# Kernel optimization log

Measured on AMD Instinct MI355X. Metric: run time of the kernel, lower is better.

Reference implementation:

```python
import jax, jax.numpy as jnp
import numpy as np

# hyperparameters (from init_kwargs)
A_LOG = 1.0
B_LOG = 1.0
C_LOG = 1.0
THR = 0.5
DT = 1.0
EPS = 1e-5


@jax.custom_vjp
def spike(v_scaled):
    # Heaviside forward, fast-sigmoid surrogate backward
    return (v_scaled > 0).astype(jnp.float32)

def _spike_fwd(v_scaled):
    return spike(v_scaled), v_scaled

def _spike_bwd(v_scaled, dy):
    return (dy / (1.0 + 100.0 * jnp.abs(v_scaled)) ** 2,)

spike.defvjp(_spike_fwd, _spike_bwd)


def setup_inputs() -> dict:
    key = jax.random.key(0)
    k1, k2, k3 = jax.random.split(key, 3)
    T, B, N_IN, N_REC = 1000, 128, 256, 256
    x = jax.random.normal(k1, (T, B, N_IN), dtype=jnp.float32)
    z0 = jnp.zeros((B, N_REC), dtype=jnp.float32)
    v0 = jnp.zeros((B, N_REC), dtype=jnp.float32)
    t0 = jnp.zeros((B, N_REC), dtype=jnp.float32)
    # RandomNormal(stddev=0.01) init for input weights
    w_in = 0.01 * jax.random.normal(k2, (N_IN, N_REC), dtype=jnp.float32)
    # recurrence enabled: small random recurrent weights
    w_rec = 0.01 * jax.random.normal(k3, (N_REC, N_REC), dtype=jnp.float32)
    return {"x": x, "z0": z0, "v0": v0, "t0": t0, "w_in": w_in, "w_rec": w_rec}


def _step(carry, x_t, w_in, w_rec):
    z, v, t = carry                              # each [B, n_rec]
    i_in = x_t @ w_in + z @ w_rec                # [B, n_rec]
    h = (i_in != 0).astype(jnp.float32)          # activity flag
    new_t = t + (1.0 - h)                        # (h != 1) == 1 - h since h in {0,1}
    new_v = v * (1.0 - z)                        # reset on spike
    low_pass = (new_v > -1.0).astype(jnp.float32)
    new_v = new_v - (1.0 - low_pass) * (new_v + 1.0)   # clamp at -1
    # logarithmic leak
    cap = (jnp.exp2(jnp.abs(new_v) / C_LOG) - B_LOG) / A_LOG
    arg = jnp.minimum(DT * h * (new_t + 1.0), cap)
    new_v = new_v - jnp.sign(new_v) * C_LOG * jnp.log2(EPS + A_LOG * arg + B_LOG)
    new_v = new_v + i_in
    new_t = new_t * (1.0 - h)
    new_z = spike((new_v - THR) / THR)
    return (new_z, new_v, new_t), (new_z, new_v)


def reference(x, z0, v0, t0, w_in, w_rec):
    def step(carry, x_t):
        return _step(carry, x_t, w_in, w_rec)
    _, (zs, vs) = jax.lax.scan(step, (z0, v0, t0), x)
    return zs, vs  # each [T, B, n_rec]
```

## Files before the change

### kernel.cpp

```cpp
#include <hip/hip_runtime.h>

__global__ __launch_bounds__(256) void gemm_xw(const float* __restrict__ X,
                                               const float* __restrict__ W,
                                               float* __restrict__ Y,
                                               int M) {
    __shared__ float As[32][132];
    __shared__ float Bs[32][128];

    const int tid = threadIdx.x;
    const int mb = blockIdx.x >> 1;
    const int nb = blockIdx.x & 1;
    const int m0 = mb << 7;
    const int n0 = nb << 7;
    const int tr = (tid >> 4) << 3;
    const int tc = (tid & 15) << 3;

    float acc[8][8];
#pragma unroll
    for (int i = 0; i < 8; ++i)
#pragma unroll
        for (int j = 0; j < 8; ++j) acc[i][j] = 0.f;

    for (int kb = 0; kb < 256; kb += 32) {
#pragma unroll
        for (int i = 0; i < 4; ++i) {
            int f = tid + (i << 8);
            int row = f >> 3, kq = f & 7;
            float4 a = *(const float4*)(X + (size_t)(m0 + row) * 256 + kb + (kq << 2));
            As[(kq << 2) + 0][row] = a.x;
            As[(kq << 2) + 1][row] = a.y;
            As[(kq << 2) + 2][row] = a.z;
            As[(kq << 2) + 3][row] = a.w;
            int rowb = f >> 5, cq = f & 31;
            *(float4*)&Bs[rowb][cq << 2] =
                *(const float4*)(W + (size_t)(kb + rowb) * 256 + n0 + (cq << 2));
        }
        __syncthreads();
#pragma unroll
        for (int k = 0; k < 32; ++k) {
            float a[8], b[8];
            *(float4*)&a[0] = *(const float4*)&As[k][tr];
            *(float4*)&a[4] = *(const float4*)&As[k][tr + 4];
            *(float4*)&b[0] = *(const float4*)&Bs[k][tc];
            *(float4*)&b[4] = *(const float4*)&Bs[k][tc + 4];
#pragma unroll
            for (int i = 0; i < 8; ++i)
#pragma unroll
                for (int j = 0; j < 8; ++j)
                    acc[i][j] = fmaf(a[i], b[j], acc[i][j]);
        }
        __syncthreads();
    }
#pragma unroll
    for (int i = 0; i < 8; ++i) {
        float* yp = Y + (size_t)(m0 + tr + i) * 256 + n0 + tc;
        *(float4*)yp = make_float4(acc[i][0], acc[i][1], acc[i][2], acc[i][3]);
        *(float4*)(yp + 4) = make_float4(acc[i][4], acc[i][5], acc[i][6], acc[i][7]);
    }
}

__global__ __launch_bounds__(64) void lif_seq(const float* __restrict__ ix,
                                              const float* __restrict__ wrec,
                                              const float* __restrict__ z0,
                                              const float* __restrict__ v0,
                                              const float* __restrict__ t0,
                                              float* __restrict__ zs,
                                              float* __restrict__ vs,
                                              int T, int B) {
    const int b = blockIdx.x;
    const int lane = threadIdx.x;
    const int nbase = lane << 2;
    const size_t sb = (size_t)b * 256 + nbase;
    const size_t stride = (size_t)B * 256;

    float4 v4 = *(const float4*)(v0 + sb);
    float4 t4 = *(const float4*)(t0 + sb);
    float4 z4 = *(const float4*)(z0 + sb);
    float v[4] = {v4.x, v4.y, v4.z, v4.w};
    float t[4] = {t4.x, t4.y, t4.z, t4.w};
    float z[4] = {z4.x, z4.y, z4.z, z4.w};

    unsigned long long mk0 = __ballot(z[0] != 0.f);
    unsigned long long mk1 = __ballot(z[1] != 0.f);
    unsigned long long mk2 = __ballot(z[2] != 0.f);
    unsigned long long mk3 = __ballot(z[3] != 0.f);

    const float* ixp = ix + sb;

    auto step = [&](int ts, float4 r) {
        float ir[4] = {0.f, 0.f, 0.f, 0.f};
        if (mk0 | mk1 | mk2 | mk3) {
            unsigned long long mm;
            mm = mk0;
            while (mm) { int j = __builtin_ctzll(mm); mm &= mm - 1;
                const float4 w = *(const float4*)(wrec + ((size_t)((j << 2) + 0) << 8) + nbase);
                ir[0] += w.x; ir[1] += w.y; ir[2] += w.z; ir[3] += w.w; }
            mm = mk1;
            while (mm) { int j = __builtin_ctzll(mm); mm &= mm - 1;
                const float4 w = *(const float4*)(wrec + ((size_t)((j << 2) + 1) << 8) + nbase);
                ir[0] += w.x; ir[1] += w.y; ir[2] += w.z; ir[3] += w.w; }
            mm = mk2;
            while (mm) { int j = __builtin_ctzll(mm); mm &= mm - 1;
                const float4 w = *(const float4*)(wrec + ((size_t)((j << 2) + 2) << 8) + nbase);
                ir[0] += w.x; ir[1] += w.y; ir[2] += w.z; ir[3] += w.w; }
            mm = mk3;
            while (mm) { int j = __builtin_ctzll(mm); mm &= mm - 1;
                const float4 w = *(const float4*)(wrec + ((size_t)((j << 2) + 3) << 8) + nbase);
                ir[0] += w.x; ir[1] += w.y; ir[2] += w.z; ir[3] += w.w; }
        }

        float rr[4] = {r.x, r.y, r.z, r.w};
        float nz[4];
#pragma unroll
        for (int c = 0; c < 4; ++c) {
            float i_in = rr[c] + ir[c];
            float h = (i_in != 0.f) ? 1.f : 0.f;
            float nt = t[c] + (1.f - h);
            float nv = (z[c] != 0.f) ? 0.f : v[c];
            nv = fmaxf(nv, -1.f);
            float cap = __builtin_amdgcn_exp2f(fabsf(nv)) - 1.f;
            float arg = fminf(h * (nt + 1.f), cap);
            float L = __builtin_amdgcn_logf((1e-5f + arg) + 1.f);
            float sgn = (nv > 0.f) ? 1.f : ((nv < 0.f) ? -1.f : 0.f);
            nv = fmaf(-sgn, L, nv);
            nv = nv + i_in;
            nt = nt * (1.f - h);
            float zn = ((nv - 0.5f) > 0.f) ? 1.f : 0.f;
            v[c] = nv; t[c] = nt; z[c] = zn; nz[c] = zn;
        }
        mk0 = __ballot(nz[0] != 0.f);
        mk1 = __ballot(nz[1] != 0.f);
        mk2 = __ballot(nz[2] != 0.f);
        mk3 = __ballot(nz[3] != 0.f);

        size_t o = (size_t)ts * stride + sb;
        *(float4*)(zs + o) = make_float4(z[0], z[1], z[2], z[3]);
        *(float4*)(vs + o) = make_float4(v[0], v[1], v[2], v[3]);
    };

    float4 bufA[8], bufB[8];

#define ISSUE(BUF, C)                                                          \
    {                                                                          \
        _Pragma("unroll") for (int u = 0; u < 8; ++u) {                        \
            const float* p_ = ixp + (size_t)((C) * 8 + u) * stride;            \
            asm volatile("global_load_dwordx4 %0, %1, off"                     \
                         : "=v"(BUF[u]) : "v"(p_) : "memory");                 \
        }                                                                      \
    }

#define RUNC(BUF, K)                                                           \
    { _Pragma("unroll") for (int u = 0; u < 8; ++u) step((K) * 8 + u, BUF[u]); }

    const int NC = T >> 3;

    ISSUE(bufA, 0);
    asm volatile("s_waitcnt vmcnt(0)" ::: "memory");
    __builtin_amdgcn_sched_barrier(0);

    for (int k = 0; k < NC; ++k) {
        asm volatile("s_waitcnt vmcnt(16)" ::: "memory");
        __builtin_amdgcn_sched_barrier(0);
        int nc1 = (k + 1 < NC) ? k + 1 : NC - 1;
        if ((k & 1) == 0) {
            ISSUE(bufB, nc1);
            RUNC(bufA, k);
        } else {
            ISSUE(bufA, nc1);
            RUNC(bufB, k);
        }
    }

    for (int ts = NC << 3; ts < T; ++ts) {
        float4 r = *(const float4*)(ixp + (size_t)ts * stride);
        step(ts, r);
    }
#undef ISSUE
#undef RUNC
}

extern "C" void kernel_launch(void* const* d_in, const int* in_sizes, int n_in,
                              void* d_out, int out_size, void* d_ws, size_t ws_size,
                              hipStream_t stream) {
    const float* x    = (const float*)d_in[0];
    const float* z0   = (const float*)d_in[1];
    const float* v0   = (const float*)d_in[2];
    const float* t0   = (const float*)d_in[3];
    const float* w_in = (const float*)d_in[4];
    const float* wrec = (const float*)d_in[5];

    const int n_rec = 256;
    const int B = in_sizes[1] / n_rec;
    const int nin = in_sizes[4] / n_rec;
    const int T = in_sizes[0] / (B * nin);
    const int M = T * B;

    float* zs = (float*)d_out;
    float* vs = zs + (size_t)T * B * n_rec;
    float* ixbuf = zs;

    gemm_xw<<<dim3((M / 128) * 2), dim3(256), 0, stream>>>(x, w_in, ixbuf, M);
    lif_seq<<<dim3(B), dim3(64), 0, stream>>>(ixbuf, wrec, z0, v0, t0, zs, vs, T, B);
}
```

Measured before the change: 550.8 us.

## Replace inline-asm prefetch pipeline with compiler-scheduled double buffering and batched stores

Drops the hand-written asm loads and explicit vmcnt waits for the input-current stream and uses plain C++ double-buffered chunk loads of 8 timesteps. Output stores are collected and issued together after each chunk. Recurrent weight loads now go through an asm load that waits on vmcnt(0) right away, which keeps the outstanding counter correct but may serialize in-flight prefetches behind every spike-driven weight load. The change trades explicit latency control for compiler scheduling.

```diff
diff --git a/kernel.cpp b/kernel.cpp
--- a/kernel.cpp
+++ b/kernel.cpp
@@ -87,30 +87,38 @@
 
     const float* ixp = ix + sb;
 
-    auto step = [&](int ts, float4 r) {
+    auto wload = [&](int row) -> float4 {
+        const float* wp = wrec + ((size_t)row << 8) + nbase;
+        float4 w4;
+        asm volatile("global_load_dwordx4 %0, %1, off\n\ts_waitcnt vmcnt(0)"
+                     : "=v"(w4) : "v"(wp) : "memory");
+        return w4;
+    };
+
+    auto step = [&](float4 r, float4& zo4, float4& vo4) {
         float ir[4] = {0.f, 0.f, 0.f, 0.f};
         if (mk0 | mk1 | mk2 | mk3) {
             unsigned long long mm;
             mm = mk0;
             while (mm) { int j = __builtin_ctzll(mm); mm &= mm - 1;
-                const float4 w = *(const float4*)(wrec + ((size_t)((j << 2) + 0) << 8) + nbase);
+                float4 w = wload((j << 2) + 0);
                 ir[0] += w.x; ir[1] += w.y; ir[2] += w.z; ir[3] += w.w; }
             mm = mk1;
             while (mm) { int j = __builtin_ctzll(mm); mm &= mm - 1;
-                const float4 w = *(const float4*)(wrec + ((size_t)((j << 2) + 1) << 8) + nbase);
+                float4 w = wload((j << 2) + 1);
                 ir[0] += w.x; ir[1] += w.y; ir[2] += w.z; ir[3] += w.w; }
             mm = mk2;
             while (mm) { int j = __builtin_ctzll(mm); mm &= mm - 1;
-                const float4 w = *(const float4*)(wrec + ((size_t)((j << 2) + 2) << 8) + nbase);
+                float4 w = wload((j << 2) + 2);
                 ir[0] += w.x; ir[1] += w.y; ir[2] += w.z; ir[3] += w.w; }
             mm = mk3;
             while (mm) { int j = __builtin_ctzll(mm); mm &= mm - 1;
-                const float4 w = *(const float4*)(wrec + ((size_t)((j << 2) + 3) << 8) + nbase);
+                float4 w = wload((j << 2) + 3);
                 ir[0] += w.x; ir[1] += w.y; ir[2] += w.z; ir[3] += w.w; }
         }
 
         float rr[4] = {r.x, r.y, r.z, r.w};
-        float nz[4];
+        float nzf[4], nvf[4];
 #pragma unroll
         for (int c = 0; c < 4; ++c) {
             float i_in = rr[c] + ir[c];
@@ -125,58 +133,62 @@
             nv = fmaf(-sgn, L, nv);
             nv = nv + i_in;
             nt = nt * (1.f - h);
-            float zn = ((nv - 0.5f) > 0.f) ? 1.f : 0.f;
-            v[c] = nv; t[c] = nt; z[c] = zn; nz[c] = zn;
-        }
-        mk0 = __ballot(nz[0] != 0.f);
-        mk1 = __ballot(nz[1] != 0.f);
-        mk2 = __ballot(nz[2] != 0.f);
-        mk3 = __ballot(nz[3] != 0.f);
-
+            float zf = ((nv - 0.5f) > 0.f) ? 1.f : 0.f;
+            v[c] = nv; t[c] = nt; z[c] = zf;
+            nvf[c] = nv; nzf[c] = zf;
+        }
+        mk0 = __ballot(nzf[0] != 0.f);
+        mk1 = __ballot(nzf[1] != 0.f);
+        mk2 = __ballot(nzf[2] != 0.f);
+        mk3 = __ballot(nzf[3] != 0.f);
+        zo4 = make_float4(nzf[0], nzf[1], nzf[2], nzf[3]);
+        vo4 = make_float4(nvf[0], nvf[1], nvf[2], nvf[3]);
+    };
+
+    float4 iA[8], iB[8];
+    float4 zo[8], vo[8];
+
+    auto loadChunk = [&](float4 (&ib)[8], int c0) {
+#pragma unroll
+        for (int u = 0; u < 8; ++u) {
+            int r = c0 + u;
+            r = (r < T) ? r : T - 1;
+            ib[u] = *(const float4*)(ixp + (size_t)r * stride);
+        }
+    };
+
+    auto runChunk = [&](float4 (&ib)[8], int c0) {
+#pragma unroll
+        for (int u = 0; u < 8; ++u) step(ib[u], zo[u], vo[u]);
+        size_t ob = (size_t)c0 * stride + sb;
+#pragma unroll
+        for (int u = 0; u < 8; ++u) {
+            *(float4*)(zs + ob + (size_t)u * stride) = zo[u];
+            *(float4*)(vs + ob + (size_t)u * stride) = vo[u];
+        }
+    };
+
+    loadChunk(iA, 0);
+    int c = 0;
+    while (c + 16 <= T) {
+        loadChunk(iB, c + 8);
+        runChunk(iA, c);
+        loadChunk(iA, c + 16);
+        runChunk(iB, c + 8);
+        c += 16;
+    }
+    if (c + 8 <= T) {
+        runChunk(iA, c);
+        c += 8;
+    }
+    for (int ts = c; ts < T; ++ts) {
+        float4 r = *(const float4*)(ixp + (size_t)ts * stride);
+        float4 zz, vv;
+        step(r, zz, vv);
         size_t o = (size_t)ts * stride + sb;
-        *(float4*)(zs + o) = make_float4(z[0], z[1], z[2], z[3]);
-        *(float4*)(vs + o) = make_float4(v[0], v[1], v[2], v[3]);
-    };
-
-    float4 bufA[8], bufB[8];
-
-#define ISSUE(BUF, C)                                                          \
-    {                                                                          \
-        _Pragma("unroll") for (int u = 0; u < 8; ++u) {                        \
-            const float* p_ = ixp + (size_t)((C) * 8 + u) * stride;            \
-            asm volatile("global_load_dwordx4 %0, %1, off"                     \
-                         : "=v"(BUF[u]) : "v"(p_) : "memory");                 \
-        }                                                                      \
-    }
-
-#define RUNC(BUF, K)                                                           \
-    { _Pragma("unroll") for (int u = 0; u < 8; ++u) step((K) * 8 + u, BUF[u]); }
-
-    const int NC = T >> 3;
-
-    ISSUE(bufA, 0);
-    asm volatile("s_waitcnt vmcnt(0)" ::: "memory");
-    __builtin_amdgcn_sched_barrier(0);
-
-    for (int k = 0; k < NC; ++k) {
-        asm volatile("s_waitcnt vmcnt(16)" ::: "memory");
-        __builtin_amdgcn_sched_barrier(0);
-        int nc1 = (k + 1 < NC) ? k + 1 : NC - 1;
-        if ((k & 1) == 0) {
-            ISSUE(bufB, nc1);
-            RUNC(bufA, k);
-        } else {
-            ISSUE(bufA, nc1);
-            RUNC(bufB, k);
-        }
-    }
-
-    for (int ts = NC << 3; ts < T; ++ts) {
-        float4 r = *(const float4*)(ixp + (size_t)ts * stride);
-        step(ts, r);
-    }
-#undef ISSUE
-#undef RUNC
+        *(float4*)(zs + o) = zz;
+        *(float4*)(vs + o) = vv;
+    }
 }
 
 extern "C" void kernel_launch(void* const* d_in, const int* in_sizes, int n_in,
```

Result: faster. 525.1 us (-4.7%).
